# Kernel optimization log

Measured on AMD Instinct MI355X. Metric: run time of the kernel, lower is better.

## Reference

```python
import jax, jax.numpy as jnp
import numpy as np

B, S, H, NH = 1, 4096, 768, 12
D = H // NH  # per-head dim = 64


def setup_inputs() -> dict:
    key = jax.random.key(0)
    ks = jax.random.split(key, 10)
    p = 0.02  # param scale
    return {
        "x": jax.random.normal(ks[0], (B, S, H), jnp.float32),
        "Wq": jax.random.normal(ks[1], (H, H), jnp.float32) * p,
        "bq": jax.random.normal(ks[2], (H,), jnp.float32) * p,
        "Wk": jax.random.normal(ks[3], (H, H), jnp.float32) * p,
        "bk": jax.random.normal(ks[4], (H,), jnp.float32) * p,
        "Wv": jax.random.normal(ks[5], (H, H), jnp.float32) * p,
        "bv": jax.random.normal(ks[6], (H,), jnp.float32) * p,
        "Wo": jax.random.normal(ks[7], (H, H), jnp.float32) * p,
        "bo": jax.random.normal(ks[8], (H,), jnp.float32) * p,
        "attn_mask": jax.random.randint(ks[9], (B, 1, 1, S), 0, 2).astype(bool),
    }


def _split_heads(t):
    # [B, S, H] -> [B, NH, S, D]
    return t.reshape(B, S, NH, D).transpose(0, 2, 1, 3)


def reference(x, Wq, bq, Wk, bk, Wv, bv, Wo, bo, attn_mask):
    q = _split_heads(x @ Wq.T + bq)
    k = _split_heads(x @ Wk.T + bk)
    v = _split_heads(x @ Wv.T + bv)
    scores = jnp.einsum('bhqd,bhkd->bhqk', q, k) / np.sqrt(D).astype(np.float32)
    scores = jnp.where(attn_mask, jnp.float32(-1e9), scores)
    attn = jax.nn.softmax(scores, axis=-1)
    ctx = jnp.einsum('bhqk,bhkd->bhqd', attn, v)
    ctx = ctx.transpose(0, 2, 1, 3).reshape(B, S, H)  # merge heads
    return ctx @ Wo.T + bo
```

## Files before the change

### kernel.cpp

```cpp
#include <hip/hip_runtime.h>
#include <stdint.h>

#define S_LEN 4096
#define HDIM  768
#define NHEAD 12
#define DHEAD 64

typedef _Float16 f16;
typedef __attribute__((ext_vector_type(8)))  _Float16 f16x8;
typedef __attribute__((ext_vector_type(4)))  _Float16 f16x4;
typedef __attribute__((ext_vector_type(4)))  float    f32x4;
typedef __attribute__((ext_vector_type(16))) float    f32x16;

typedef __attribute__((address_space(1))) void gv_t;
typedef __attribute__((address_space(3))) void lv_t;

__device__ __forceinline__ void async_copy16(const void* g, void* l) {
  __builtin_amdgcn_global_load_lds((gv_t*)g, (lv_t*)l, 16, 0, 0);
}

__device__ __forceinline__ float fast_exp2(float x) {
#if __has_builtin(__builtin_amdgcn_exp2f)
  return __builtin_amdgcn_exp2f(x);
#else
  return exp2f(x);
#endif
}

__device__ __forceinline__ int swz4(int row) { return (row ^ (row >> 2)) & 3; }

constexpr size_t OFF_META = 0;
constexpr size_t OFF_POS  = 256;
constexpr size_t OFF_XB   = 65536;
constexpr size_t SZ_XB    = (size_t)S_LEN * HDIM * 2;
constexpr size_t OFF_WQKV = OFF_XB + SZ_XB;
constexpr size_t SZ_WQKV  = (size_t)3 * HDIM * HDIM * 2;
constexpr size_t OFF_WO   = OFF_WQKV + SZ_WQKV;
constexpr size_t SZ_WO    = (size_t)HDIM * HDIM * 2;
constexpr size_t OFF_Q    = OFF_WO + SZ_WO;
constexpr size_t SZ_HD    = (size_t)NHEAD * S_LEN * DHEAD * 2;
constexpr size_t OFF_K    = OFF_Q + SZ_HD;
constexpr size_t OFF_VT   = OFF_K + SZ_HD;
constexpr size_t OFF_VR   = OFF_VT + SZ_HD;
constexpr size_t OFF_PO1  = OFF_VR + SZ_HD;

__global__ __launch_bounds__(256) void k_prep(const float* __restrict__ x,
                                              const float* __restrict__ wq,
                                              const float* __restrict__ wk,
                                              const float* __restrict__ wv,
                                              const float* __restrict__ wo,
                                              const int* __restrict__ mi,
                                              f16* __restrict__ dst,
                                              f16* __restrict__ Kc,
                                              int* __restrict__ pos,
                                              int* __restrict__ meta) {
  __shared__ int s_flag;
  __shared__ int s_cnt[256];
  const int b = blockIdx.x, tid = threadIdx.x;
  if (b < 5376) {
    int i = b * 256 + tid;
    const float* src; int off;
    if (i < 786432) { src = x; off = i; }
    else {
      int j = i - 786432;
      int w = j / 147456;
      off = j - w * 147456;
      src = (w == 0) ? wq : (w == 1) ? wk : (w == 2) ? wv : wo;
    }
    float4 v = ((const float4*)src)[off];
    f16x4 h;
    h[0] = (f16)v.x; h[1] = (f16)v.y; h[2] = (f16)v.z; h[3] = (f16)v.w;
    ((f16x4*)dst)[i] = h;
    return;
  }
  if (b < 6144) {
    int u = (b - 5376) * 512 + tid;
    f16x8 z = {};
    ((f16x8*)Kc)[u] = z;
    ((f16x8*)Kc)[u + 256] = z;
    return;
  }
  if (tid == 0) s_flag = 1;
  __syncthreads();
  int bad = 0;
  #pragma unroll
  for (int k = 0; k < 4; ++k) {
    int v = mi[k * 256 + tid];
    if (v != 0 && v != 1) bad = 1;
  }
  if (bad) atomicAnd(&s_flag, 0);
  __syncthreads();
  const int isInt = s_flag;
  const unsigned char* mu8 = (const unsigned char*)mi;
  int keep[16]; int cnt = 0;
  const int s0 = tid * 16;
  #pragma unroll
  for (int k = 0; k < 16; ++k) {
    int mval = isInt ? mi[s0 + k] : (int)mu8[s0 + k];
    keep[k] = (mval == 0) ? 1 : 0;
    cnt += keep[k];
  }
  s_cnt[tid] = cnt;
  __syncthreads();
  for (int off = 1; off < 256; off <<= 1) {
    int t = (tid >= off) ? s_cnt[tid - off] : 0;
    __syncthreads();
    s_cnt[tid] += t;
    __syncthreads();
  }
  int base = s_cnt[tid] - cnt;
  #pragma unroll
  for (int k = 0; k < 16; ++k) {
    pos[s0 + k] = keep[k] ? base : -1;
    base += keep[k];
  }
  if (tid == 255) meta[0] = s_cnt[255];
}

__global__ __launch_bounds__(256) void k_qkv(
    const f16* __restrict__ xb, const f16* __restrict__ wqkv,
    const float* __restrict__ bq, const float* __restrict__ bk, const float* __restrict__ bv,
    const int* __restrict__ pos,
    f16* __restrict__ Qh, f16* __restrict__ Kc, f16* __restrict__ Vrow) {
  __shared__ __attribute__((aligned(16))) f16 lA[128 * 32];
  __shared__ __attribute__((aligned(16))) f16 lB[128 * 32];
  const int tid = threadIdx.x;
  const int wid = tid >> 6, lane = tid & 63;
  const int hf = lane >> 5, l31 = lane & 31;
  const int wm = wid >> 1, wn = wid & 1;
  const int tn = blockIdx.x;
  const int m0 = blockIdx.y * 128;
  const int mat = tn / 6;
  const int nb = (tn % 6) * 128;
  const f16* wbase = wqkv + (size_t)mat * HDIM * HDIM;

  f32x16 acc[2][2] = {};

  for (int k0 = 0; k0 < HDIM; k0 += 32) {
    #pragma unroll
    for (int iss = 0; iss < 2; ++iss) {
      int c = iss * 256 + tid;
      int row = c >> 2, slot = c & 3;
      int gs = slot ^ swz4(row);
      async_copy16((const char*)(xb + (size_t)(m0 + row) * HDIM + k0) + gs * 16,
                   (char*)lA + (iss * 256 + wid * 64) * 16);
      async_copy16((const char*)(wbase + (size_t)(nb + row) * HDIM + k0) + gs * 16,
                   (char*)lB + (iss * 256 + wid * 64) * 16);
    }
    __syncthreads();
    #pragma unroll
    for (int kk = 0; kk < 2; ++kk) {
      f16x8 af[2], bf[2];
      #pragma unroll
      for (int mi = 0; mi < 2; ++mi) {
        int row = wm * 64 + mi * 32 + l31;
        af[mi] = *(const f16x8*)&lA[row * 32 + (((kk * 2 + hf) ^ swz4(row)) * 8)];
      }
      #pragma unroll
      for (int ni = 0; ni < 2; ++ni) {
        int row = wn * 64 + ni * 32 + l31;
        bf[ni] = *(const f16x8*)&lB[row * 32 + (((kk * 2 + hf) ^ swz4(row)) * 8)];
      }
      #pragma unroll
      for (int mi = 0; mi < 2; ++mi)
        #pragma unroll
        for (int ni = 0; ni < 2; ++ni)
          acc[mi][ni] = __builtin_amdgcn_mfma_f32_32x32x16_f16(af[mi], bf[ni], acc[mi][ni], 0, 0, 0);
    }
    __syncthreads();
  }

  const float* bias = (mat == 0) ? bq : (mat == 1) ? bk : bv;
  const float qscale = 0.125f * 1.44269504088896341f;
  f16* kvdst = (mat == 1) ? Kc : Vrow;
  #pragma unroll
  for (int mi = 0; mi < 2; ++mi) {
    #pragma unroll
    for (int ni = 0; ni < 2; ++ni) {
      int n = nb + wn * 64 + ni * 32 + l31;
      int head = n >> 6, d = n & 63;
      float b = bias[n];
      #pragma unroll
      for (int reg = 0; reg < 16; ++reg) {
        int s = m0 + wm * 64 + mi * 32 + (reg & 3) + 8 * (reg >> 2) + 4 * hf;
        float val = acc[mi][ni][reg] + b;
        if (mat == 0) {
          Qh[((size_t)head * S_LEN + s) * DHEAD + d] = (f16)(val * qscale);
        } else {
          int p = pos[s];
          if (p >= 0)
            kvdst[((size_t)head * S_LEN + p) * DHEAD + d] = (f16)val;
        }
      }
    }
  }
}

__global__ __launch_bounds__(256) void k_vt(const int* __restrict__ meta,
                                            const f16* __restrict__ Vrow,
                                            f16* __restrict__ Vtc) {
  const int kc = meta[0];
  const int kcp = (kc + 63) & ~63;
  const int p0 = blockIdx.x * 64;
  const int h = blockIdx.y;
  if (p0 >= kcp) return;
  __shared__ __attribute__((aligned(16))) f16 lT[64 * 80];
  const int tid = threadIdx.x;
  for (int u = tid; u < 512; u += 256) {
    int d8 = u >> 6, p = u & 63;
    f16x8 v = {};
    if (p0 + p < kc) v = *(const f16x8*)&Vrow[((size_t)h * S_LEN + p0 + p) * DHEAD + d8 * 8];
    #pragma unroll
    for (int j = 0; j < 8; ++j) lT[(d8 * 8 + j) * 80 + p] = v[j];
  }
  __syncthreads();
  for (int w = tid; w < 512; w += 256) {
    int d = w >> 3, p8 = w & 7;
    int base16 = (p8 >> 1) * 16, half = p8 & 1;
    f16x4 lo = *(const f16x4*)&lT[d * 80 + base16 + half * 4];
    f16x4 hi = *(const f16x4*)&lT[d * 80 + base16 + 8 + half * 4];
    f16x8 o;
    o[0] = lo[0]; o[1] = lo[1]; o[2] = lo[2]; o[3] = lo[3];
    o[4] = hi[0]; o[5] = hi[1]; o[6] = hi[2]; o[7] = hi[3];
    *(f16x8*)&Vtc[((size_t)h * DHEAD + d) * S_LEN + p0 + p8 * 8] = o;
  }
}

__global__ __launch_bounds__(256, 3) void k_attn(
    const f16* __restrict__ Qh, const f16* __restrict__ Kc, const f16* __restrict__ Vtc,
    const int* __restrict__ meta, f16* __restrict__ PO0, f16* __restrict__ PO1,
    float* __restrict__ PL) {
  __shared__ __attribute__((aligned(16))) f16 lK[64 * 64];
  __shared__ __attribute__((aligned(16))) f16 lV[64 * 64];
  const int tid = threadIdx.x;
  const int wid = tid >> 6, lane = tid & 63;
  const int hf = lane >> 5, l31 = lane & 31, r7 = l31 & 7;
  const int id = blockIdx.x;
  const int xcd = id & 7;
  const int j = id >> 3;
  const int pair = xcd * 3 + (j >> 5);
  const int head = pair >> 1;
  const int split = pair & 1;
  const int q0 = (j & 31) * 128 + wid * 32;
  const int kc = meta[0];
  const int nkt = (kc + 63) >> 6;
  const int th = nkt >> 1;
  const int t0 = split ? th : 0;
  const int t1 = split ? nkt : th;

  const f16* Qp = Qh + ((size_t)head * S_LEN + q0 + l31) * DHEAD;
  f16x8 qf[4];
  #pragma unroll
  for (int dc = 0; dc < 4; ++dc) qf[dc] = *(const f16x8*)(Qp + dc * 16 + hf * 8);

  f32x16 accO[2] = {};
  float lsum = 0.f;

  const char* kbase = (const char*)(Kc + (size_t)head * S_LEN * DHEAD);
  const char* vbase = (const char*)(Vtc + (size_t)head * DHEAD * S_LEN);

  for (int t = t0; t < t1; ++t) {
    const int j0 = t * 64;
    #pragma unroll
    for (int iss = 0; iss < 2; ++iss) {
      int c = iss * 256 + tid;
      int row = c >> 3, slot = c & 7;
      int gs = slot ^ (row & 7);
      async_copy16(kbase + (size_t)(j0 + row) * 128 + gs * 16,
                   (char*)lK + (iss * 256 + wid * 64) * 16);
      async_copy16(vbase + (size_t)row * (S_LEN * 2) + (size_t)j0 * 2 + gs * 16,
                   (char*)lV + (iss * 256 + wid * 64) * 16);
    }
    __syncthreads();

    #pragma unroll
    for (int mh = 0; mh < 2; ++mh) {
      f16x8 af[4];
      const int arow = mh * 32 + l31;
      #pragma unroll
      for (int dc = 0; dc < 4; ++dc)
        af[dc] = *(const f16x8*)&lK[arow * 64 + ((((dc << 1) | hf) ^ r7) * 8)];
      f32x16 s = {};
      #pragma unroll
      for (int dc = 0; dc < 4; ++dc)
        s = __builtin_amdgcn_mfma_f32_32x32x16_f16(af[dc], qf[dc], s, 0, 0, 0);
      #pragma unroll
      for (int u = 0; u < 16; ++u) { s[u] = fast_exp2(s[u]); lsum += s[u]; }
      #pragma unroll
      for (int cc = 0; cc < 2; ++cc) {
        f16x8 pf;
        #pragma unroll
        for (int u = 0; u < 8; ++u) pf[u] = (f16)s[8 * cc + u];
        const int c2 = mh * 2 + cc;
        #pragma unroll
        for (int dh = 0; dh < 2; ++dh) {
          const int vrow = dh * 32 + l31;
          f16x8 vf = *(const f16x8*)&lV[vrow * 64 + ((((c2 << 1) | hf) ^ r7) * 8)];
          accO[dh] = __builtin_amdgcn_mfma_f32_32x32x16_f16(pf, vf, accO[dh], 0, 0, 0);
        }
      }
    }
    __syncthreads();
  }

  lsum += __shfl_xor(lsum, 32);
  if (split == 1) lsum -= (float)(nkt * 64 - kc);
  if (hf == 0)
    PL[((size_t)split * NHEAD + head) * S_LEN + q0 + l31] = lsum;

  f16* PO = split ? PO1 : PO0;
  #pragma unroll
  for (int dh = 0; dh < 2; ++dh)
    #pragma unroll
    for (int reg = 0; reg < 16; ++reg) {
      int row = (reg & 3) + 8 * (reg >> 2) + 4 * hf;
      PO[((size_t)head * S_LEN + q0 + row) * DHEAD + dh * 32 + l31] = (f16)accO[dh][reg];
    }
}

__global__ __launch_bounds__(256) void k_out(
    const f16* __restrict__ PO0, const f16* __restrict__ PO1,
    const float* __restrict__ PL, const f16* __restrict__ wo,
    const float* __restrict__ bo, float* __restrict__ out) {
  __shared__ __attribute__((aligned(16))) f16 lA[128 * 32];
  __shared__ __attribute__((aligned(16))) f16 lB[128 * 32];
  __shared__ float linv[NHEAD * 128];
  const int tid = threadIdx.x;
  const int wid = tid >> 6, lane = tid & 63;
  const int hf = lane >> 5, l31 = lane & 31;
  const int wm = wid >> 1, wn = wid & 1;
  const int nb = blockIdx.x * 128;
  const int m0 = blockIdx.y * 128;

  for (int i = tid; i < NHEAD * 128; i += 256) {
    int h = i >> 7, r = i & 127;
    float l = PL[(size_t)h * S_LEN + m0 + r] + PL[(size_t)(NHEAD + h) * S_LEN + m0 + r];
    linv[i] = 1.0f / l;
  }
  __syncthreads();

  f32x16 acc[2][2] = {};

  for (int k0 = 0; k0 < HDIM; k0 += 32) {
    const int head = k0 >> 6, d0 = k0 & 63;
    #pragma unroll
    for (int iss = 0; iss < 2; ++iss) {
      int c = iss * 256 + tid;
      int row = c >> 2, slot = c & 3;
      int gs = slot ^ swz4(row);
      size_t pi = ((size_t)head * S_LEN + m0 + row) * DHEAD + d0 + gs * 8;
      f16x8 a0 = *(const f16x8*)(PO0 + pi);
      f16x8 a1 = *(const f16x8*)(PO1 + pi);
      float il = linv[head * 128 + row];
      f16x8 av;
      #pragma unroll
      for (int u = 0; u < 8; ++u) av[u] = (f16)(((float)a0[u] + (float)a1[u]) * il);
      *(f16x8*)&lA[c * 8] = av;
      async_copy16((const char*)(wo + (size_t)(nb + row) * HDIM + k0) + gs * 16,
                   (char*)lB + (iss * 256 + wid * 64) * 16);
    }
    __syncthreads();
    #pragma unroll
    for (int kk = 0; kk < 2; ++kk) {
      f16x8 af[2], bf[2];
      #pragma unroll
      for (int mi = 0; mi < 2; ++mi) {
        int row = wm * 64 + mi * 32 + l31;
        af[mi] = *(const f16x8*)&lA[row * 32 + (((kk * 2 + hf) ^ swz4(row)) * 8)];
      }
      #pragma unroll
      for (int ni = 0; ni < 2; ++ni) {
        int row = wn * 64 + ni * 32 + l31;
        bf[ni] = *(const f16x8*)&lB[row * 32 + (((kk * 2 + hf) ^ swz4(row)) * 8)];
      }
      #pragma unroll
      for (int mi = 0; mi < 2; ++mi)
        #pragma unroll
        for (int ni = 0; ni < 2; ++ni)
          acc[mi][ni] = __builtin_amdgcn_mfma_f32_32x32x16_f16(af[mi], bf[ni], acc[mi][ni], 0, 0, 0);
    }
    __syncthreads();
  }

  #pragma unroll
  for (int mi = 0; mi < 2; ++mi) {
    #pragma unroll
    for (int ni = 0; ni < 2; ++ni) {
      int n = nb + wn * 64 + ni * 32 + l31;
      float b = bo[n];
      #pragma unroll
      for (int reg = 0; reg < 16; ++reg) {
        int s = m0 + wm * 64 + mi * 32 + (reg & 3) + 8 * (reg >> 2) + 4 * hf;
        out[(size_t)s * HDIM + n] = acc[mi][ni][reg] + b;
      }
    }
  }
}

extern "C" void kernel_launch(void* const* d_in, const int* in_sizes, int n_in,
                              void* d_out, int out_size, void* d_ws, size_t ws_size,
                              hipStream_t stream) {
  const float* x  = (const float*)d_in[0];
  const float* Wq = (const float*)d_in[1];
  const float* bq = (const float*)d_in[2];
  const float* Wk = (const float*)d_in[3];
  const float* bk = (const float*)d_in[4];
  const float* Wv = (const float*)d_in[5];
  const float* bv = (const float*)d_in[6];
  const float* Wo = (const float*)d_in[7];
  const float* bo = (const float*)d_in[8];
  const int*   mask = (const int*)d_in[9];
  float* out = (float*)d_out;

  char* ws = (char*)d_ws;
  int* meta  = (int*)(ws + OFF_META);
  int* pos   = (int*)(ws + OFF_POS);
  f16* xb    = (f16*)(ws + OFF_XB);
  f16* wqkv  = (f16*)(ws + OFF_WQKV);
  f16* wob   = (f16*)(ws + OFF_WO);
  f16* Qh    = (f16*)(ws + OFF_Q);
  f16* Kc    = (f16*)(ws + OFF_K);
  f16* Vtc   = (f16*)(ws + OFF_VT);
  f16* Vrow  = (f16*)(ws + OFF_VR);
  f16* PO0   = (f16*)(ws + OFF_VR);
  f16* PO1   = (f16*)(ws + OFF_PO1);
  float* PL  = (float*)(ws + OFF_WQKV);

  k_prep<<<dim3(6145), 256, 0, stream>>>(x, Wq, Wk, Wv, Wo, mask, xb, Kc, pos, meta);
  k_qkv<<<dim3(18, 32), 256, 0, stream>>>(xb, wqkv, bq, bk, bv, pos, Qh, Kc, Vrow);
  k_vt<<<dim3(64, NHEAD), 256, 0, stream>>>(meta, Vrow, Vtc);
  k_attn<<<dim3(768), 256, 0, stream>>>(Qh, Kc, Vtc, meta, PO0, PO1, PL);
  k_out<<<dim3(6, 32), 256, 0, stream>>>(PO0, PO1, PL, wob, bo, out);
}
```

Before: 190.6 us.

## Double-buffer K/V LDS tiles in attention and switch to a 3D grid

The attention kernel now keeps two LDS buffers for K and V. It prefetches the next key tile with async global-to-LDS copies while the current tile is used for MFMA compute, which needs only one barrier per iteration instead of two. The aim is to hide global load latency behind the QK and PV matrix ops. The launch also drops the XCD-aware block index remapping in favor of a plain (q-block, head, split) grid. That can spread one head's K/V across XCD L2 caches and reduce cache reuse. LDS use doubles to 32KB per block.

```diff
diff --git a/kernel.cpp b/kernel.cpp
--- a/kernel.cpp
+++ b/kernel.cpp
@@ -230,18 +230,14 @@
     const f16* __restrict__ Qh, const f16* __restrict__ Kc, const f16* __restrict__ Vtc,
     const int* __restrict__ meta, f16* __restrict__ PO0, f16* __restrict__ PO1,
     float* __restrict__ PL) {
-  __shared__ __attribute__((aligned(16))) f16 lK[64 * 64];
-  __shared__ __attribute__((aligned(16))) f16 lV[64 * 64];
+  __shared__ __attribute__((aligned(16))) f16 lK[2][64 * 64];
+  __shared__ __attribute__((aligned(16))) f16 lV[2][64 * 64];
   const int tid = threadIdx.x;
   const int wid = tid >> 6, lane = tid & 63;
   const int hf = lane >> 5, l31 = lane & 31, r7 = l31 & 7;
-  const int id = blockIdx.x;
-  const int xcd = id & 7;
-  const int j = id >> 3;
-  const int pair = xcd * 3 + (j >> 5);
-  const int head = pair >> 1;
-  const int split = pair & 1;
-  const int q0 = (j & 31) * 128 + wid * 32;
+  const int head = blockIdx.y;
+  const int split = blockIdx.z;
+  const int q0 = blockIdx.x * 128 + wid * 32;
   const int kc = meta[0];
   const int nkt = (kc + 63) >> 6;
   const int th = nkt >> 1;
@@ -258,20 +254,27 @@
 
   const char* kbase = (const char*)(Kc + (size_t)head * S_LEN * DHEAD);
   const char* vbase = (const char*)(Vtc + (size_t)head * DHEAD * S_LEN);
-
+  const int srow = tid >> 3, sslot = tid & 7;
+
+  #define STAGE(t, b)                                                                   \
+    do {                                                                                \
+      const int j0_ = (t) * 64;                                                         \
+      _Pragma("unroll")                                                                 \
+      for (int iss = 0; iss < 2; ++iss) {                                               \
+        int row_ = iss * 32 + srow;                                                     \
+        int gs_ = sslot ^ (row_ & 7);                                                   \
+        async_copy16(kbase + (size_t)(j0_ + row_) * 128 + gs_ * 16,                     \
+                     (char*)&lK[b][0] + (iss * 256 + wid * 64) * 16);                   \
+        async_copy16(vbase + (size_t)row_ * (S_LEN * 2) + (size_t)j0_ * 2 + gs_ * 16,   \
+                     (char*)&lV[b][0] + (iss * 256 + wid * 64) * 16);                   \
+      }                                                                                 \
+    } while (0)
+
+  STAGE(t0, 0);
   for (int t = t0; t < t1; ++t) {
-    const int j0 = t * 64;
-    #pragma unroll
-    for (int iss = 0; iss < 2; ++iss) {
-      int c = iss * 256 + tid;
-      int row = c >> 3, slot = c & 7;
-      int gs = slot ^ (row & 7);
-      async_copy16(kbase + (size_t)(j0 + row) * 128 + gs * 16,
-                   (char*)lK + (iss * 256 + wid * 64) * 16);
-      async_copy16(vbase + (size_t)row * (S_LEN * 2) + (size_t)j0 * 2 + gs * 16,
-                   (char*)lV + (iss * 256 + wid * 64) * 16);
-    }
-    __syncthreads();
+    const int b = (t - t0) & 1;
+    __syncthreads();
+    if (t + 1 < t1) STAGE(t + 1, b ^ 1);
 
     #pragma unroll
     for (int mh = 0; mh < 2; ++mh) {
@@ -279,7 +282,7 @@
       const int arow = mh * 32 + l31;
       #pragma unroll
       for (int dc = 0; dc < 4; ++dc)
-        af[dc] = *(const f16x8*)&lK[arow * 64 + ((((dc << 1) | hf) ^ r7) * 8)];
+        af[dc] = *(const f16x8*)&lK[b][arow * 64 + ((((dc << 1) | hf) ^ r7) * 8)];
       f32x16 s = {};
       #pragma unroll
       for (int dc = 0; dc < 4; ++dc)
@@ -295,13 +298,13 @@
         #pragma unroll
         for (int dh = 0; dh < 2; ++dh) {
           const int vrow = dh * 32 + l31;
-          f16x8 vf = *(const f16x8*)&lV[vrow * 64 + ((((c2 << 1) | hf) ^ r7) * 8)];
+          f16x8 vf = *(const f16x8*)&lV[b][vrow * 64 + ((((c2 << 1) | hf) ^ r7) * 8)];
           accO[dh] = __builtin_amdgcn_mfma_f32_32x32x16_f16(pf, vf, accO[dh], 0, 0, 0);
         }
       }
     }
-    __syncthreads();
-  }
+  }
+  #undef STAGE
 
   lsum += __shfl_xor(lsum, 32);
   if (split == 1) lsum -= (float)(nkt * 64 - kc);
@@ -429,6 +432,6 @@
   k_prep<<<dim3(6145), 256, 0, stream>>>(x, Wq, Wk, Wv, Wo, mask, xb, Kc, pos, meta);
   k_qkv<<<dim3(18, 32), 256, 0, stream>>>(xb, wqkv, bq, bk, bv, pos, Qh, Kc, Vrow);
   k_vt<<<dim3(64, NHEAD), 256, 0, stream>>>(meta, Vrow, Vtc);
-  k_attn<<<dim3(768), 256, 0, stream>>>(Qh, Kc, Vtc, meta, PO0, PO1, PL);
+  k_attn<<<dim3(32, NHEAD, 2), 256, 0, stream>>>(Qh, Kc, Vtc, meta, PO0, PO1, PL);
   k_out<<<dim3(6, 32), 256, 0, stream>>>(PO0, PO1, PL, wob, bo, out);
 }
```

New measurement: 190.3 us. No clear change (-0.2%).

## Split attention keys four ways and zero only padded K rows

Applied to the files above, without the earlier changes.

Attention now splits the compacted key range into four chunks instead of two. It launches a 3D grid of query tile × head × split, and occupancy is raised to four blocks per CU. The output projection kernel sums four partial numerators and row sums before normalising. The full zero-fill of the compacted K buffer in the prep kernel is dropped; k_vt now zeroes only the tail rows past the valid key count. The goal is more parallel work per CU and less memory traffic, at the cost of more partial-output reads and writes, a larger workspace footprint, and losing the XCD-aware block remapping.

```diff
diff --git a/kernel.cpp b/kernel.cpp
--- a/kernel.cpp
+++ b/kernel.cpp
@@ -5,6 +5,7 @@
 #define HDIM  768
 #define NHEAD 12
 #define DHEAD 64
+#define NSPLIT 4
 
 typedef _Float16 f16;
 typedef __attribute__((ext_vector_type(8)))  _Float16 f16x8;
@@ -51,7 +52,6 @@
                                               const float* __restrict__ wo,
                                               const int* __restrict__ mi,
                                               f16* __restrict__ dst,
-                                              f16* __restrict__ Kc,
                                               int* __restrict__ pos,
                                               int* __restrict__ meta) {
   __shared__ int s_flag;
@@ -71,13 +71,6 @@
     f16x4 h;
     h[0] = (f16)v.x; h[1] = (f16)v.y; h[2] = (f16)v.z; h[3] = (f16)v.w;
     ((f16x4*)dst)[i] = h;
-    return;
-  }
-  if (b < 6144) {
-    int u = (b - 5376) * 512 + tid;
-    f16x8 z = {};
-    ((f16x8*)Kc)[u] = z;
-    ((f16x8*)Kc)[u + 256] = z;
     return;
   }
   if (tid == 0) s_flag = 1;
@@ -198,14 +191,23 @@
 
 __global__ __launch_bounds__(256) void k_vt(const int* __restrict__ meta,
                                             const f16* __restrict__ Vrow,
-                                            f16* __restrict__ Vtc) {
+                                            f16* __restrict__ Vtc,
+                                            f16* __restrict__ Kc) {
   const int kc = meta[0];
   const int kcp = (kc + 63) & ~63;
   const int p0 = blockIdx.x * 64;
   const int h = blockIdx.y;
+  const int tid = threadIdx.x;
   if (p0 >= kcp) return;
+  if (p0 <= kc && kc < p0 + 64 && kc < kcp) {
+    const int npad = kcp - kc;
+    for (int u = tid; u < npad * 8; u += 256) {
+      int r = kc + (u >> 3), c8 = u & 7;
+      f16x8 z = {};
+      *(f16x8*)&Kc[((size_t)h * S_LEN + r) * DHEAD + c8 * 8] = z;
+    }
+  }
   __shared__ __attribute__((aligned(16))) f16 lT[64 * 80];
-  const int tid = threadIdx.x;
   for (int u = tid; u < 512; u += 256) {
     int d8 = u >> 6, p = u & 63;
     f16x8 v = {};
@@ -226,27 +228,21 @@
   }
 }
 
-__global__ __launch_bounds__(256, 3) void k_attn(
+__global__ __launch_bounds__(256, 4) void k_attn(
     const f16* __restrict__ Qh, const f16* __restrict__ Kc, const f16* __restrict__ Vtc,
-    const int* __restrict__ meta, f16* __restrict__ PO0, f16* __restrict__ PO1,
-    float* __restrict__ PL) {
+    const int* __restrict__ meta, f16* __restrict__ POb, float* __restrict__ PL) {
   __shared__ __attribute__((aligned(16))) f16 lK[64 * 64];
   __shared__ __attribute__((aligned(16))) f16 lV[64 * 64];
   const int tid = threadIdx.x;
   const int wid = tid >> 6, lane = tid & 63;
   const int hf = lane >> 5, l31 = lane & 31, r7 = l31 & 7;
-  const int id = blockIdx.x;
-  const int xcd = id & 7;
-  const int j = id >> 3;
-  const int pair = xcd * 3 + (j >> 5);
-  const int head = pair >> 1;
-  const int split = pair & 1;
-  const int q0 = (j & 31) * 128 + wid * 32;
+  const int head = blockIdx.y;
+  const int split = blockIdx.z;
+  const int q0 = blockIdx.x * 128 + wid * 32;
   const int kc = meta[0];
   const int nkt = (kc + 63) >> 6;
-  const int th = nkt >> 1;
-  const int t0 = split ? th : 0;
-  const int t1 = split ? nkt : th;
+  const int t0 = (split * nkt) >> 2;
+  const int t1 = ((split + 1) * nkt) >> 2;
 
   const f16* Qp = Qh + ((size_t)head * S_LEN + q0 + l31) * DHEAD;
   f16x8 qf[4];
@@ -304,11 +300,11 @@
   }
 
   lsum += __shfl_xor(lsum, 32);
-  if (split == 1) lsum -= (float)(nkt * 64 - kc);
+  if (split == NSPLIT - 1) lsum -= (float)(nkt * 64 - kc);
   if (hf == 0)
     PL[((size_t)split * NHEAD + head) * S_LEN + q0 + l31] = lsum;
 
-  f16* PO = split ? PO1 : PO0;
+  f16* PO = POb + (size_t)split * NHEAD * S_LEN * DHEAD;
   #pragma unroll
   for (int dh = 0; dh < 2; ++dh)
     #pragma unroll
@@ -319,9 +315,8 @@
 }
 
 __global__ __launch_bounds__(256) void k_out(
-    const f16* __restrict__ PO0, const f16* __restrict__ PO1,
-    const float* __restrict__ PL, const f16* __restrict__ wo,
-    const float* __restrict__ bo, float* __restrict__ out) {
+    const f16* __restrict__ POb, const float* __restrict__ PL,
+    const f16* __restrict__ wo, const float* __restrict__ bo, float* __restrict__ out) {
   __shared__ __attribute__((aligned(16))) f16 lA[128 * 32];
   __shared__ __attribute__((aligned(16))) f16 lB[128 * 32];
   __shared__ float linv[NHEAD * 128];
@@ -331,10 +326,14 @@
   const int wm = wid >> 1, wn = wid & 1;
   const int nb = blockIdx.x * 128;
   const int m0 = blockIdx.y * 128;
+  constexpr size_t POSTRIDE = (size_t)NHEAD * S_LEN * DHEAD;
 
   for (int i = tid; i < NHEAD * 128; i += 256) {
     int h = i >> 7, r = i & 127;
-    float l = PL[(size_t)h * S_LEN + m0 + r] + PL[(size_t)(NHEAD + h) * S_LEN + m0 + r];
+    float l = 0.f;
+    #pragma unroll
+    for (int sp = 0; sp < NSPLIT; ++sp)
+      l += PL[((size_t)sp * NHEAD + h) * S_LEN + m0 + r];
     linv[i] = 1.0f / l;
   }
   __syncthreads();
@@ -349,12 +348,17 @@
       int row = c >> 2, slot = c & 3;
       int gs = slot ^ swz4(row);
       size_t pi = ((size_t)head * S_LEN + m0 + row) * DHEAD + d0 + gs * 8;
-      f16x8 a0 = *(const f16x8*)(PO0 + pi);
-      f16x8 a1 = *(const f16x8*)(PO1 + pi);
+      float sum[8] = {};
+      #pragma unroll
+      for (int sp = 0; sp < NSPLIT; ++sp) {
+        f16x8 a = *(const f16x8*)(POb + sp * POSTRIDE + pi);
+        #pragma unroll
+        for (int u = 0; u < 8; ++u) sum[u] += (float)a[u];
+      }
       float il = linv[head * 128 + row];
       f16x8 av;
       #pragma unroll
-      for (int u = 0; u < 8; ++u) av[u] = (f16)(((float)a0[u] + (float)a1[u]) * il);
+      for (int u = 0; u < 8; ++u) av[u] = (f16)(sum[u] * il);
       *(f16x8*)&lA[c * 8] = av;
       async_copy16((const char*)(wo + (size_t)(nb + row) * HDIM + k0) + gs * 16,
                    (char*)lB + (iss * 256 + wid * 64) * 16);
@@ -422,13 +426,12 @@
   f16* Kc    = (f16*)(ws + OFF_K);
   f16* Vtc   = (f16*)(ws + OFF_VT);
   f16* Vrow  = (f16*)(ws + OFF_VR);
-  f16* PO0   = (f16*)(ws + OFF_VR);
-  f16* PO1   = (f16*)(ws + OFF_PO1);
+  f16* POb   = (f16*)(ws + OFF_VR);
   float* PL  = (float*)(ws + OFF_WQKV);
 
-  k_prep<<<dim3(6145), 256, 0, stream>>>(x, Wq, Wk, Wv, Wo, mask, xb, Kc, pos, meta);
+  k_prep<<<dim3(5377), 256, 0, stream>>>(x, Wq, Wk, Wv, Wo, mask, xb, pos, meta);
   k_qkv<<<dim3(18, 32), 256, 0, stream>>>(xb, wqkv, bq, bk, bv, pos, Qh, Kc, Vrow);
-  k_vt<<<dim3(64, NHEAD), 256, 0, stream>>>(meta, Vrow, Vtc);
-  k_attn<<<dim3(768), 256, 0, stream>>>(Qh, Kc, Vtc, meta, PO0, PO1, PL);
-  k_out<<<dim3(6, 32), 256, 0, stream>>>(PO0, PO1, PL, wob, bo, out);
-}
+  k_vt<<<dim3(64, NHEAD), 256, 0, stream>>>(meta, Vrow, Vtc, Kc);
+  k_attn<<<dim3(32, NHEAD, NSPLIT), 256, 0, stream>>>(Qh, Kc, Vtc, meta, POb, PL);
+  k_out<<<dim3(6, 32), 256, 0, stream>>>(POb, PL, wob, bo, out);
+}
```

Result: slower. 204.3 us (+7.2%).

## Gather unmasked rows before K/V projection and skip masked-row GEMM tiles

Applied to the files above, without the earlier changes.

The prep kernel now builds a compacted list of unmasked row indices instead of a per-row position map. The K/V projection gathers only those rows of x as its A operand and exits early for tiles beyond the kept count, so masked keys are never projected. The zero-padding of Kc moves from a full-buffer clear in prep to a small tail fill in the V-transpose kernel. The attention grid also drops the XCD-aware block remapping in favour of a plain 3D grid, which may change cache locality across chiplets.

```diff
diff --git a/kernel.cpp b/kernel.cpp
--- a/kernel.cpp
+++ b/kernel.cpp
@@ -30,7 +30,7 @@
 __device__ __forceinline__ int swz4(int row) { return (row ^ (row >> 2)) & 3; }
 
 constexpr size_t OFF_META = 0;
-constexpr size_t OFF_POS  = 256;
+constexpr size_t OFF_RIDX = 256;
 constexpr size_t OFF_XB   = 65536;
 constexpr size_t SZ_XB    = (size_t)S_LEN * HDIM * 2;
 constexpr size_t OFF_WQKV = OFF_XB + SZ_XB;
@@ -51,8 +51,7 @@
                                               const float* __restrict__ wo,
                                               const int* __restrict__ mi,
                                               f16* __restrict__ dst,
-                                              f16* __restrict__ Kc,
-                                              int* __restrict__ pos,
+                                              int* __restrict__ ridx,
                                               int* __restrict__ meta) {
   __shared__ int s_flag;
   __shared__ int s_cnt[256];
@@ -73,13 +72,6 @@
     ((f16x4*)dst)[i] = h;
     return;
   }
-  if (b < 6144) {
-    int u = (b - 5376) * 512 + tid;
-    f16x8 z = {};
-    ((f16x8*)Kc)[u] = z;
-    ((f16x8*)Kc)[u + 256] = z;
-    return;
-  }
   if (tid == 0) s_flag = 1;
   __syncthreads();
   int bad = 0;
@@ -99,6 +91,7 @@
     int mval = isInt ? mi[s0 + k] : (int)mu8[s0 + k];
     keep[k] = (mval == 0) ? 1 : 0;
     cnt += keep[k];
+    ridx[s0 + k] = 0;
   }
   s_cnt[tid] = cnt;
   __syncthreads();
@@ -111,8 +104,7 @@
   int base = s_cnt[tid] - cnt;
   #pragma unroll
   for (int k = 0; k < 16; ++k) {
-    pos[s0 + k] = keep[k] ? base : -1;
-    base += keep[k];
+    if (keep[k]) { ridx[base] = s0 + k; ++base; }
   }
   if (tid == 255) meta[0] = s_cnt[255];
 }
@@ -120,7 +112,7 @@
 __global__ __launch_bounds__(256) void k_qkv(
     const f16* __restrict__ xb, const f16* __restrict__ wqkv,
     const float* __restrict__ bq, const float* __restrict__ bk, const float* __restrict__ bv,
-    const int* __restrict__ pos,
+    const int* __restrict__ ridx, const int* __restrict__ meta,
     f16* __restrict__ Qh, f16* __restrict__ Kc, f16* __restrict__ Vrow) {
   __shared__ __attribute__((aligned(16))) f16 lA[128 * 32];
   __shared__ __attribute__((aligned(16))) f16 lB[128 * 32];
@@ -132,21 +124,35 @@
   const int m0 = blockIdx.y * 128;
   const int mat = tn / 6;
   const int nb = (tn % 6) * 128;
+  const int kc = meta[0];
+  if (mat != 0 && m0 >= kc) return;
   const f16* wbase = wqkv + (size_t)mat * HDIM * HDIM;
 
+  const int ar0 = tid >> 2, ar1 = 64 + (tid >> 2);
+  const f16* asrc0;
+  const f16* asrc1;
+  if (mat == 0) {
+    asrc0 = xb + (size_t)(m0 + ar0) * HDIM;
+    asrc1 = xb + (size_t)(m0 + ar1) * HDIM;
+  } else {
+    int g0 = (m0 + ar0 < kc) ? ridx[m0 + ar0] : 0;
+    int g1 = (m0 + ar1 < kc) ? ridx[m0 + ar1] : 0;
+    asrc0 = xb + (size_t)g0 * HDIM;
+    asrc1 = xb + (size_t)g1 * HDIM;
+  }
+  const int slot = tid & 3;
+  const int gs0 = slot ^ swz4(ar0);
+  const int gs1 = slot ^ swz4(ar1);
+
   f32x16 acc[2][2] = {};
 
   for (int k0 = 0; k0 < HDIM; k0 += 32) {
-    #pragma unroll
-    for (int iss = 0; iss < 2; ++iss) {
-      int c = iss * 256 + tid;
-      int row = c >> 2, slot = c & 3;
-      int gs = slot ^ swz4(row);
-      async_copy16((const char*)(xb + (size_t)(m0 + row) * HDIM + k0) + gs * 16,
-                   (char*)lA + (iss * 256 + wid * 64) * 16);
-      async_copy16((const char*)(wbase + (size_t)(nb + row) * HDIM + k0) + gs * 16,
-                   (char*)lB + (iss * 256 + wid * 64) * 16);
-    }
+    async_copy16((const char*)(asrc0 + k0) + gs0 * 16, (char*)lA + (wid * 64) * 16);
+    async_copy16((const char*)(asrc1 + k0) + gs1 * 16, (char*)lA + (256 + wid * 64) * 16);
+    async_copy16((const char*)(wbase + (size_t)(nb + ar0) * HDIM + k0) + gs0 * 16,
+                 (char*)lB + (wid * 64) * 16);
+    async_copy16((const char*)(wbase + (size_t)(nb + ar1) * HDIM + k0) + gs1 * 16,
+                 (char*)lB + (256 + wid * 64) * 16);
     __syncthreads();
     #pragma unroll
     for (int kk = 0; kk < 2; ++kk) {
@@ -186,10 +192,8 @@
         float val = acc[mi][ni][reg] + b;
         if (mat == 0) {
           Qh[((size_t)head * S_LEN + s) * DHEAD + d] = (f16)(val * qscale);
-        } else {
-          int p = pos[s];
-          if (p >= 0)
-            kvdst[((size_t)head * S_LEN + p) * DHEAD + d] = (f16)val;
+        } else if (s < kc) {
+          kvdst[((size_t)head * S_LEN + s) * DHEAD + d] = (f16)val;
         }
       }
     }
@@ -198,14 +202,23 @@
 
 __global__ __launch_bounds__(256) void k_vt(const int* __restrict__ meta,
                                             const f16* __restrict__ Vrow,
-                                            f16* __restrict__ Vtc) {
+                                            f16* __restrict__ Vtc,
+                                            f16* __restrict__ Kc) {
   const int kc = meta[0];
   const int kcp = (kc + 63) & ~63;
   const int p0 = blockIdx.x * 64;
   const int h = blockIdx.y;
+  const int tid = threadIdx.x;
   if (p0 >= kcp) return;
+  if (p0 <= kc && kc < p0 + 64 && kc < kcp) {
+    const int npad = kcp - kc;
+    for (int u = tid; u < npad * 8; u += 256) {
+      int r = kc + (u >> 3), c8 = u & 7;
+      f16x8 z = {};
+      *(f16x8*)&Kc[((size_t)h * S_LEN + r) * DHEAD + c8 * 8] = z;
+    }
+  }
   __shared__ __attribute__((aligned(16))) f16 lT[64 * 80];
-  const int tid = threadIdx.x;
   for (int u = tid; u < 512; u += 256) {
     int d8 = u >> 6, p = u & 63;
     f16x8 v = {};
@@ -235,13 +248,9 @@
   const int tid = threadIdx.x;
   const int wid = tid >> 6, lane = tid & 63;
   const int hf = lane >> 5, l31 = lane & 31, r7 = l31 & 7;
-  const int id = blockIdx.x;
-  const int xcd = id & 7;
-  const int j = id >> 3;
-  const int pair = xcd * 3 + (j >> 5);
-  const int head = pair >> 1;
-  const int split = pair & 1;
-  const int q0 = (j & 31) * 128 + wid * 32;
+  const int head = blockIdx.y;
+  const int split = blockIdx.z;
+  const int q0 = blockIdx.x * 128 + wid * 32;
   const int kc = meta[0];
   const int nkt = (kc + 63) >> 6;
   const int th = nkt >> 1;
@@ -414,7 +423,7 @@
 
   char* ws = (char*)d_ws;
   int* meta  = (int*)(ws + OFF_META);
-  int* pos   = (int*)(ws + OFF_POS);
+  int* ridx  = (int*)(ws + OFF_RIDX);
   f16* xb    = (f16*)(ws + OFF_XB);
   f16* wqkv  = (f16*)(ws + OFF_WQKV);
   f16* wob   = (f16*)(ws + OFF_WO);
@@ -426,9 +435,9 @@
   f16* PO1   = (f16*)(ws + OFF_PO1);
   float* PL  = (float*)(ws + OFF_WQKV);
 
-  k_prep<<<dim3(6145), 256, 0, stream>>>(x, Wq, Wk, Wv, Wo, mask, xb, Kc, pos, meta);
-  k_qkv<<<dim3(18, 32), 256, 0, stream>>>(xb, wqkv, bq, bk, bv, pos, Qh, Kc, Vrow);
-  k_vt<<<dim3(64, NHEAD), 256, 0, stream>>>(meta, Vrow, Vtc);
-  k_attn<<<dim3(768), 256, 0, stream>>>(Qh, Kc, Vtc, meta, PO0, PO1, PL);
+  k_prep<<<dim3(5377), 256, 0, stream>>>(x, Wq, Wk, Wv, Wo, mask, xb, ridx, meta);
+  k_qkv<<<dim3(18, 32), 256, 0, stream>>>(xb, wqkv, bq, bk, bv, ridx, meta, Qh, Kc, Vrow);
+  k_vt<<<dim3(64, NHEAD), 256, 0, stream>>>(meta, Vrow, Vtc, Kc);
+  k_attn<<<dim3(32, NHEAD, 2), 256, 0, stream>>>(Qh, Kc, Vtc, meta, PO0, PO1, PL);
   k_out<<<dim3(6, 32), 256, 0, stream>>>(PO0, PO1, PL, wob, bo, out);
 }
```

New measurement: 182.2 us. 4.4% less time.
